# Performance work log

Hardware: AMD Instinct MI355X
Metric: run time of the kernel (lower is better)

Reference implementation:

```python
import jax, jax.numpy as jnp
from jax import lax
import numpy as np

B, H, W, C = 64, 224, 224, 3
OH, OW = 224, 224
EPS = 1e-3  # keras BatchNormalization default epsilon
FLAT = 52 * 52 * 10  # after conv7(valid)->pool2->conv5(valid)->pool2 on 224x224


def setup_inputs() -> dict:
    key = jax.random.key(0)
    ks = jax.random.split(key, 6)
    return {
        "x": jax.random.normal(ks[0], (B, H, W, C), jnp.float32),
        "c1_w": jax.random.normal(ks[1], (7, 7, C, 8), jnp.float32) * 0.05,
        "c1_b": jnp.zeros((8,), jnp.float32),
        "g1": jnp.ones((8,), jnp.float32),
        "b1": jnp.zeros((8,), jnp.float32),
        "m1": jnp.zeros((8,), jnp.float32),
        "v1": jnp.ones((8,), jnp.float32),
        "c2_w": jax.random.normal(ks[2], (5, 5, 8, 10), jnp.float32) * 0.05,
        "c2_b": jnp.zeros((10,), jnp.float32),
        "g2": jnp.ones((10,), jnp.float32),
        "b2": jnp.zeros((10,), jnp.float32),
        "m2": jnp.zeros((10,), jnp.float32),
        "v2": jnp.ones((10,), jnp.float32),
        "d1_w": jax.random.normal(ks[3], (FLAT, 32), jnp.float32) * 0.01,
        "d1_b": jnp.zeros((32,), jnp.float32),
        "d2_w": jax.random.normal(ks[4], (32, 6), jnp.float32) * 0.01,
        "d2_b": jnp.array([1.0, 0.0, 0.0, 0.0, 1.0, 0.0], jnp.float32),  # identity affine
    }


def _conv(x, w, b):
    return lax.conv_general_dilated(x, w, (1, 1), 'VALID',
                                    dimension_numbers=('NHWC', 'HWIO', 'NHWC')) + b


def _maxpool(x):
    return lax.reduce_window(x, -jnp.inf, lax.max, (1, 2, 2, 1), (1, 2, 2, 1), 'VALID')


def _bn(x, g, b, m, v):
    # inference-mode batchnorm: gamma*(x-mean)/sqrt(var+eps)+beta
    return (x - m) * lax.rsqrt(v + EPS) * g + b


def _bilinear(img, px, py):
    # img: [H,W,C]; px,py: [OH,OW] pixel-space sample coords; zero fill outside
    x0 = jnp.floor(px).astype(jnp.int32)
    y0 = jnp.floor(py).astype(jnp.int32)

    def gather(yi, xi):
        valid = (yi >= 0) & (yi < H) & (xi >= 0) & (xi < W)
        v = img[jnp.clip(yi, 0, H - 1), jnp.clip(xi, 0, W - 1)]  # [OH,OW,C]
        return v * valid[..., None]

    wx = (px - x0)[..., None]
    wy = (py - y0)[..., None]
    return (gather(y0, x0) * (1 - wx) * (1 - wy)
            + gather(y0, x0 + 1) * wx * (1 - wy)
            + gather(y0 + 1, x0) * (1 - wx) * wy
            + gather(y0 + 1, x0 + 1) * wx * wy)


def reference(x, c1_w, c1_b, g1, b1, m1, v1, c2_w, c2_b, g2, b2, m2, v2,
              d1_w, d1_b, d2_w, d2_b):
    # localization network
    h = _maxpool(_bn(jax.nn.relu(_conv(x, c1_w, c1_b)), g1, b1, m1, v1))
    h = _maxpool(_bn(jax.nn.relu(_conv(h, c2_w, c2_b)), g2, b2, m2, v2))
    h = h.reshape(h.shape[0], -1)                      # [B, FLAT]
    h = jax.nn.relu(h @ d1_w + d1_b)                   # [B, 32]
    theta = (h @ d2_w + d2_b).reshape(-1, 2, 3)        # [B, 2, 3]

    # normalized homogeneous grid [N,3] with N = OH*OW
    xs = jnp.linspace(-1.0, 1.0, OW)
    ys = jnp.linspace(-1.0, 1.0, OH)
    xg, yg = jnp.meshgrid(xs, ys)
    grid = jnp.stack([xg.ravel(), yg.ravel(), jnp.ones(OH * OW, jnp.float32)], axis=-1)

    coords = jnp.einsum('bij,nj->bni', theta, grid)    # [B, N, 2]
    px = ((coords[..., 0] + 1.0) * 0.5 * (W - 1)).reshape(-1, OH, OW)
    py = ((coords[..., 1] + 1.0) * 0.5 * (H - 1)).reshape(-1, OH, OW)
    return jax.vmap(_bilinear)(x, px, py)              # [B, OH, OW, C]
```

## Files before the change

### kernel.cpp

```cpp
#include <hip/hip_runtime.h>
#include <hip/hip_bf16.h>


#define NCHUNK 212
#define KC 128

__global__ __launch_bounds__(256) void k_conv1(
    const float* __restrict__ x, const float* __restrict__ w,
    const float* __restrict__ bias, const float* __restrict__ g,
    const float* __restrict__ bt, const float* __restrict__ m,
    const float* __restrict__ v, float* __restrict__ out) {
  __shared__ float s_in[3][38][42];
  __shared__ float s_bn[3][8];
  const int tid = threadIdx.x;
  const int bx = blockIdx.x, by = blockIdx.y, b = blockIdx.z;

  if (tid < 8) {
    float sc = g[tid] * rsqrtf(v[tid] + 1e-3f);
    s_bn[0][tid] = sc;
    s_bn[1][tid] = bt[tid] - m[tid] * sc;
    s_bn[2][tid] = bias[tid];
  }
  const int iy0 = by * 32, ix0 = bx * 32;
  const float* xb = x + (size_t)b * 224 * 224 * 3;
  for (int f = tid; f < 38 * 114; f += 256) {
    int r = f / 114, rem = f - r * 114;
    int q = rem / 3, c = rem - q * 3;
    int gy = iy0 + r; if (gy > 223) gy = 223;
    int gc = ix0 + q; if (gc > 223) gc = 223;
    s_in[c][r][q] = xb[(gy * 224 + gc) * 3 + c];
  }
  __syncthreads();

  const int pxl = tid & 15, pyl = tid >> 4;
  const int lx = 2 * pxl, ly = 2 * pyl;
  float acc[2][2][8];
#pragma unroll
  for (int pr = 0; pr < 2; ++pr)
#pragma unroll
    for (int pc = 0; pc < 2; ++pc)
#pragma unroll
      for (int co = 0; co < 8; ++co) acc[pr][pc][co] = 0.f;

#pragma unroll 1
  for (int ci = 0; ci < 3; ++ci) {
    float rw[8][8];
#pragma unroll
    for (int r = 0; r < 8; ++r)
#pragma unroll
      for (int j = 0; j < 4; ++j) {
        float2 t = *(const float2*)&s_in[ci][ly + r][lx + 2 * j];
        rw[r][2 * j] = t.x; rw[r][2 * j + 1] = t.y;
      }
#pragma unroll
    for (int ky = 0; ky < 7; ++ky) {
      float wv[7][8];
#pragma unroll
      for (int kx = 0; kx < 7; ++kx) {
        const float* wp = w + ((ky * 7 + kx) * 3 + ci) * 8;
        float4 a = *(const float4*)wp;
        float4 c4 = *(const float4*)(wp + 4);
        wv[kx][0] = a.x;  wv[kx][1] = a.y;  wv[kx][2] = a.z;  wv[kx][3] = a.w;
        wv[kx][4] = c4.x; wv[kx][5] = c4.y; wv[kx][6] = c4.z; wv[kx][7] = c4.w;
      }
#pragma unroll
      for (int kx = 0; kx < 7; ++kx)
#pragma unroll
        for (int pr = 0; pr < 2; ++pr)
#pragma unroll
          for (int pc = 0; pc < 2; ++pc) {
            float iv = rw[ky + pr][kx + pc];
#pragma unroll
            for (int co = 0; co < 8; ++co)
              acc[pr][pc][co] = fmaf(iv, wv[kx][co], acc[pr][pc][co]);
          }
    }
  }

  const int py = by * 16 + pyl, px = bx * 16 + pxl;
  if (py < 109 && px < 109) {
#pragma unroll
    for (int co = 0; co < 8; ++co) {
      float sc = s_bn[0][co], sh = s_bn[1][co], bs = s_bn[2][co];
      float a0 = fmaxf(acc[0][0][co] + bs, 0.f) * sc + sh;
      float a1 = fmaxf(acc[0][1][co] + bs, 0.f) * sc + sh;
      float a2 = fmaxf(acc[1][0][co] + bs, 0.f) * sc + sh;
      float a3 = fmaxf(acc[1][1][co] + bs, 0.f) * sc + sh;
      out[((size_t)co * 64 + b) * 109 * 110 + py * 110 + px] =
          fmaxf(fmaxf(a0, a1), fmaxf(a2, a3));
    }
  }
}

__global__ __launch_bounds__(256) void k_conv2(
    const float* __restrict__ in, const float* __restrict__ w,
    const float* __restrict__ bias, const float* __restrict__ g,
    const float* __restrict__ bt, const float* __restrict__ m,
    const float* __restrict__ v, float* __restrict__ out) {
  __shared__ float s_in[8][36][38];
  __shared__ float s_bn[3][10];
  const int tid = threadIdx.x;
  const int bx = blockIdx.x, by = blockIdx.y, b = blockIdx.z;

  if (tid < 10) {
    float sc = g[tid] * rsqrtf(v[tid] + 1e-3f);
    s_bn[0][tid] = sc;
    s_bn[1][tid] = bt[tid] - m[tid] * sc;
    s_bn[2][tid] = bias[tid];
  }
  const int iy0 = by * 32, ix0 = bx * 32;
  for (int f = tid; f < 8 * 36 * 36; f += 256) {
    int ci = f / 1296, rem = f - ci * 1296;
    int r = rem / 36, q = rem - r * 36;
    int gy = iy0 + r; if (gy > 108) gy = 108;
    int gc = ix0 + q; if (gc > 108) gc = 108;
    s_in[ci][r][q] = in[(((size_t)ci * 64 + b) * 109 + gy) * 110 + gc];
  }
  __syncthreads();

  const int pxl = tid & 15, pyl = tid >> 4;
  const int lx = 2 * pxl, ly = 2 * pyl;
  float acc[2][2][10];
#pragma unroll
  for (int pr = 0; pr < 2; ++pr)
#pragma unroll
    for (int pc = 0; pc < 2; ++pc)
#pragma unroll
      for (int co = 0; co < 10; ++co) acc[pr][pc][co] = 0.f;

#pragma unroll 1
  for (int ci = 0; ci < 8; ++ci) {
    float rw[6][8];
#pragma unroll
    for (int r = 0; r < 6; ++r)
#pragma unroll
      for (int j = 0; j < 4; ++j) {
        float2 t = *(const float2*)&s_in[ci][ly + r][lx + 2 * j];
        rw[r][2 * j] = t.x; rw[r][2 * j + 1] = t.y;
      }
#pragma unroll
    for (int ky = 0; ky < 5; ++ky) {
      float wv[5][10];
#pragma unroll
      for (int kx = 0; kx < 5; ++kx) {
        const float* wp = w + ((ky * 5 + kx) * 8 + ci) * 10;
#pragma unroll
        for (int u = 0; u < 5; ++u) {
          float2 t = *(const float2*)(wp + 2 * u);
          wv[kx][2 * u] = t.x; wv[kx][2 * u + 1] = t.y;
        }
      }
#pragma unroll
      for (int kx = 0; kx < 5; ++kx)
#pragma unroll
        for (int pr = 0; pr < 2; ++pr)
#pragma unroll
          for (int pc = 0; pc < 2; ++pc) {
            float iv = rw[ky + pr][kx + pc];
#pragma unroll
            for (int co = 0; co < 10; ++co)
              acc[pr][pc][co] = fmaf(iv, wv[kx][co], acc[pr][pc][co]);
          }
    }
  }

  const int py = by * 16 + pyl, px = bx * 16 + pxl;
  if (py < 52 && px < 52) {
    float res[10];
#pragma unroll
    for (int co = 0; co < 10; ++co) {
      float sc = s_bn[0][co], sh = s_bn[1][co], bs = s_bn[2][co];
      float a0 = fmaxf(acc[0][0][co] + bs, 0.f) * sc + sh;
      float a1 = fmaxf(acc[0][1][co] + bs, 0.f) * sc + sh;
      float a2 = fmaxf(acc[1][0][co] + bs, 0.f) * sc + sh;
      float a3 = fmaxf(acc[1][1][co] + bs, 0.f) * sc + sh;
      res[co] = fmaxf(fmaxf(a0, a1), fmaxf(a2, a3));
    }
    float2* op2 = (float2*)&out[(((size_t)b * 52 + py) * 52 + px) * 10];
#pragma unroll
    for (int i = 0; i < 5; i++)
      op2[i] = make_float2(res[2 * i], res[2 * i + 1]);
  }
}

__global__ __launch_bounds__(256) void k_fc1(
    const float* __restrict__ act, const float* __restrict__ w,
    float* __restrict__ partial) {
  __shared__ float s_w[KC * 32];
  __shared__ float s_a[64 * KC];
  const int tid = threadIdx.x;
  const int chunk = blockIdx.x;
  const int k0 = chunk * KC;
  for (int f = tid; f < KC * 32; f += 256) {
    int k = k0 + (f >> 5);
    s_w[f] = (k < 27040) ? w[(size_t)k0 * 32 + f] : 0.f;
  }
  for (int f = tid; f < 64 * KC; f += 256) {
    int bb = f >> 7, j = f & (KC - 1);
    int k = k0 + j;
    s_a[f] = (k < 27040) ? act[(size_t)bb * 27040 + k] : 0.f;
  }
  __syncthreads();
  const int o = tid & 31, bh = tid >> 5;
  float sums[8];
#pragma unroll
  for (int i = 0; i < 8; i++) sums[i] = 0.f;
#pragma unroll 1
  for (int j = 0; j < KC; j++) {
    float wv = s_w[j * 32 + o];
#pragma unroll
    for (int i = 0; i < 8; i++)
      sums[i] = fmaf(s_a[(i * 8 + bh) * KC + j], wv, sums[i]);
  }
#pragma unroll
  for (int i = 0; i < 8; i++)
    partial[(size_t)chunk * 2048 + i * 256 + tid] = sums[i];
}

__global__ __launch_bounds__(64) void k_fc2(
    const float* __restrict__ partial, const float* __restrict__ d1b,
    const float* __restrict__ d2w, const float* __restrict__ d2b,
    float* __restrict__ theta) {
  const int b = blockIdx.x;
  const int t = threadIdx.x;
  const int o = t & 31, half = t >> 5;
  float s = 0.f;
  const int c0 = half * (NCHUNK / 2), c1 = c0 + (NCHUNK / 2);
#pragma unroll 4
  for (int c = c0; c < c1; c++)
    s += partial[(size_t)c * 2048 + b * 32 + o];
  s += __shfl_down(s, 32);
  __shared__ float s_h[32];
  if (t < 32) s_h[o] = fmaxf(s + d1b[o], 0.f);
  __syncthreads();
  if (t < 6) {
    float th = d2b[t];
#pragma unroll
    for (int o2 = 0; o2 < 32; o2++) th = fmaf(s_h[o2], d2w[o2 * 6 + t], th);
    theta[b * 6 + t] = th;
  }
}

__global__ __launch_bounds__(256) void k_sample(
    const float* __restrict__ x, const float* __restrict__ theta,
    float* __restrict__ out) {
  const int b = blockIdx.y;
  __shared__ float th[6];
  if (threadIdx.x < 6) th[threadIdx.x] = theta[b * 6 + threadIdx.x];
  __syncthreads();
  const int t = blockIdx.x * 256 + threadIdx.x;
  const int oy = t / 224, ox = t - oy * 224;
  const float xn = -1.f + (2.f / 223.f) * (float)ox;
  const float yn = -1.f + (2.f / 223.f) * (float)oy;
  const float cx = th[0] * xn + th[1] * yn + th[2];
  const float cy = th[3] * xn + th[4] * yn + th[5];
  const float px = (cx + 1.f) * 0.5f * 223.f;
  const float py = (cy + 1.f) * 0.5f * 223.f;
  const float x0f = floorf(px), y0f = floorf(py);
  const int x0 = (int)x0f, y0 = (int)y0f;
  const float wx = px - x0f, wy = py - y0f;
  const float* xb = x + (size_t)b * 224 * 224 * 3;
  float a0 = 0.f, a1 = 0.f, a2 = 0.f;
#pragma unroll
  for (int dy = 0; dy < 2; dy++) {
    const int yi = y0 + dy;
    const bool vy = (yi >= 0) && (yi < 224);
    const int yc = yi < 0 ? 0 : (yi > 223 ? 223 : yi);
    const float wyv = dy ? wy : 1.f - wy;
#pragma unroll
    for (int dx = 0; dx < 2; dx++) {
      const int xi = x0 + dx;
      const bool vx = (xi >= 0) && (xi < 224);
      const int xc = xi < 0 ? 0 : (xi > 223 ? 223 : xi);
      const float wv = wyv * (dx ? wx : 1.f - wx) * ((vx && vy) ? 1.f : 0.f);
      const float* p = &xb[(yc * 224 + xc) * 3];
      a0 = fmaf(p[0], wv, a0);
      a1 = fmaf(p[1], wv, a1);
      a2 = fmaf(p[2], wv, a2);
    }
  }
  float* op = &out[((size_t)b * 50176 + t) * 3];
  op[0] = a0; op[1] = a1; op[2] = a2;
}

extern "C" void kernel_launch(void* const* d_in, const int* in_sizes, int n_in,
                              void* d_out, int out_size, void* d_ws, size_t ws_size,
                              hipStream_t stream) {
  const float* x    = (const float*)d_in[0];
  const float* c1w  = (const float*)d_in[1];
  const float* c1b  = (const float*)d_in[2];
  const float* g1   = (const float*)d_in[3];
  const float* b1   = (const float*)d_in[4];
  const float* m1   = (const float*)d_in[5];
  const float* v1   = (const float*)d_in[6];
  const float* c2w  = (const float*)d_in[7];
  const float* c2b  = (const float*)d_in[8];
  const float* g2   = (const float*)d_in[9];
  const float* b2   = (const float*)d_in[10];
  const float* m2   = (const float*)d_in[11];
  const float* v2   = (const float*)d_in[12];
  const float* d1w  = (const float*)d_in[13];
  const float* d1b  = (const float*)d_in[14];
  const float* d2w  = (const float*)d_in[15];
  const float* d2b  = (const float*)d_in[16];
  float* out = (float*)d_out;

  float* ws = (float*)d_ws;
  float* p1    = ws;
  float* p2    = p1 + 6138880;
  float* theta = p2 + 1730560;
  float* part  = ws;

  k_conv1<<<dim3(7, 7, 64), 256, 0, stream>>>(x, c1w, c1b, g1, b1, m1, v1, p1);
  k_conv2<<<dim3(4, 4, 64), 256, 0, stream>>>(p1, c2w, c2b, g2, b2, m2, v2, p2);
  k_fc1<<<NCHUNK, 256, 0, stream>>>(p2, d1w, part);
  k_fc2<<<64, 64, 0, stream>>>(part, d1b, d2w, d2b, theta);
  k_sample<<<dim3(196, 64), 256, 0, stream>>>(x, theta, out);
}
```

Baseline: 295.4 us.

## Process two images per conv1 block and retile FC1 reduction with vectorized loads

conv1 now handles two batch images per block, so each weight register load is reused across both images. Input rows are now loaded per ky rather than all at once, which cuts register pressure; launch bounds request 4 waves per SIMD. fc1 uses half-size K chunks (twice as many blocks) with float4 shared-memory reads and a new partial-sum layout, and fc2 reduces across 8 warp segments through shared memory. The risk is higher accumulator register use in conv1 and fewer conv1 blocks.

```diff
diff --git a/kernel.cpp b/kernel.cpp
--- a/kernel.cpp
+++ b/kernel.cpp
@@ -2,18 +2,19 @@
 #include <hip/hip_bf16.h>
 
 
-#define NCHUNK 212
-#define KC 128
-
-__global__ __launch_bounds__(256) void k_conv1(
+#define NCHUNK 423
+#define KC 64
+
+__global__ __launch_bounds__(256, 4) void k_conv1(
     const float* __restrict__ x, const float* __restrict__ w,
     const float* __restrict__ bias, const float* __restrict__ g,
     const float* __restrict__ bt, const float* __restrict__ m,
     const float* __restrict__ v, float* __restrict__ out) {
-  __shared__ float s_in[3][38][42];
+  __shared__ float s_in[2][3][38][42];
   __shared__ float s_bn[3][8];
   const int tid = threadIdx.x;
-  const int bx = blockIdx.x, by = blockIdx.y, b = blockIdx.z;
+  const int bx = blockIdx.x, by = blockIdx.y, z = blockIdx.z;
+  const int b0 = 2 * z;
 
   if (tid < 8) {
     float sc = g[tid] * rsqrtf(v[tid] + 1e-3f);
@@ -22,38 +23,40 @@
     s_bn[2][tid] = bias[tid];
   }
   const int iy0 = by * 32, ix0 = bx * 32;
-  const float* xb = x + (size_t)b * 224 * 224 * 3;
-  for (int f = tid; f < 38 * 114; f += 256) {
-    int r = f / 114, rem = f - r * 114;
-    int q = rem / 3, c = rem - q * 3;
+  for (int f = tid; f < 2 * 38 * 114; f += 256) {
+    int img = f / 4332, rem = f - img * 4332;
+    int r = rem / 114, rem2 = rem - r * 114;
+    int q = rem2 / 3, c = rem2 - q * 3;
     int gy = iy0 + r; if (gy > 223) gy = 223;
     int gc = ix0 + q; if (gc > 223) gc = 223;
-    s_in[c][r][q] = xb[(gy * 224 + gc) * 3 + c];
+    s_in[img][c][r][q] = x[((size_t)(b0 + img) * 224 + gy) * 224 * 3 + gc * 3 + c];
   }
   __syncthreads();
 
   const int pxl = tid & 15, pyl = tid >> 4;
   const int lx = 2 * pxl, ly = 2 * pyl;
-  float acc[2][2][8];
+  float accA[2][2][8], accB[2][2][8];
 #pragma unroll
   for (int pr = 0; pr < 2; ++pr)
 #pragma unroll
     for (int pc = 0; pc < 2; ++pc)
 #pragma unroll
-      for (int co = 0; co < 8; ++co) acc[pr][pc][co] = 0.f;
+      for (int co = 0; co < 8; ++co) { accA[pr][pc][co] = 0.f; accB[pr][pc][co] = 0.f; }
 
 #pragma unroll 1
   for (int ci = 0; ci < 3; ++ci) {
-    float rw[8][8];
-#pragma unroll
-    for (int r = 0; r < 8; ++r)
-#pragma unroll
-      for (int j = 0; j < 4; ++j) {
-        float2 t = *(const float2*)&s_in[ci][ly + r][lx + 2 * j];
-        rw[r][2 * j] = t.x; rw[r][2 * j + 1] = t.y;
-      }
-#pragma unroll
+#pragma unroll 1
     for (int ky = 0; ky < 7; ++ky) {
+      float rA[2][8], rB[2][8];
+#pragma unroll
+      for (int rr = 0; rr < 2; ++rr)
+#pragma unroll
+        for (int j = 0; j < 4; ++j) {
+          float2 ta = *(const float2*)&s_in[0][ci][ly + ky + rr][lx + 2 * j];
+          rA[rr][2 * j] = ta.x; rA[rr][2 * j + 1] = ta.y;
+          float2 tb = *(const float2*)&s_in[1][ci][ly + ky + rr][lx + 2 * j];
+          rB[rr][2 * j] = tb.x; rB[rr][2 * j + 1] = tb.y;
+        }
       float wv[7][8];
 #pragma unroll
       for (int kx = 0; kx < 7; ++kx) {
@@ -69,10 +72,13 @@
         for (int pr = 0; pr < 2; ++pr)
 #pragma unroll
           for (int pc = 0; pc < 2; ++pc) {
-            float iv = rw[ky + pr][kx + pc];
-#pragma unroll
-            for (int co = 0; co < 8; ++co)
-              acc[pr][pc][co] = fmaf(iv, wv[kx][co], acc[pr][pc][co]);
+            float ia = rA[pr][kx + pc];
+            float ib = rB[pr][kx + pc];
+#pragma unroll
+            for (int co = 0; co < 8; ++co) {
+              accA[pr][pc][co] = fmaf(ia, wv[kx][co], accA[pr][pc][co]);
+              accB[pr][pc][co] = fmaf(ib, wv[kx][co], accB[pr][pc][co]);
+            }
           }
     }
   }
@@ -82,12 +88,18 @@
 #pragma unroll
     for (int co = 0; co < 8; ++co) {
       float sc = s_bn[0][co], sh = s_bn[1][co], bs = s_bn[2][co];
-      float a0 = fmaxf(acc[0][0][co] + bs, 0.f) * sc + sh;
-      float a1 = fmaxf(acc[0][1][co] + bs, 0.f) * sc + sh;
-      float a2 = fmaxf(acc[1][0][co] + bs, 0.f) * sc + sh;
-      float a3 = fmaxf(acc[1][1][co] + bs, 0.f) * sc + sh;
-      out[((size_t)co * 64 + b) * 109 * 110 + py * 110 + px] =
+      float a0 = fmaxf(accA[0][0][co] + bs, 0.f) * sc + sh;
+      float a1 = fmaxf(accA[0][1][co] + bs, 0.f) * sc + sh;
+      float a2 = fmaxf(accA[1][0][co] + bs, 0.f) * sc + sh;
+      float a3 = fmaxf(accA[1][1][co] + bs, 0.f) * sc + sh;
+      out[((size_t)co * 64 + b0) * 109 * 110 + py * 110 + px] =
           fmaxf(fmaxf(a0, a1), fmaxf(a2, a3));
+      float c0 = fmaxf(accB[0][0][co] + bs, 0.f) * sc + sh;
+      float c1 = fmaxf(accB[0][1][co] + bs, 0.f) * sc + sh;
+      float c2 = fmaxf(accB[1][0][co] + bs, 0.f) * sc + sh;
+      float c3 = fmaxf(accB[1][1][co] + bs, 0.f) * sc + sh;
+      out[((size_t)co * 64 + b0 + 1) * 109 * 110 + py * 110 + px] =
+          fmaxf(fmaxf(c0, c1), fmaxf(c2, c3));
     }
   }
 }
@@ -186,52 +198,67 @@
 __global__ __launch_bounds__(256) void k_fc1(
     const float* __restrict__ act, const float* __restrict__ w,
     float* __restrict__ partial) {
+  __shared__ float s_a[64][KC];
   __shared__ float s_w[KC * 32];
-  __shared__ float s_a[64 * KC];
   const int tid = threadIdx.x;
   const int chunk = blockIdx.x;
   const int k0 = chunk * KC;
+  for (int f = tid; f < 64 * KC; f += 256) {
+    int row = f >> 6, j = f & (KC - 1);
+    int k = k0 + j;
+    s_a[row][j] = (k < 27040) ? act[(size_t)row * 27040 + k] : 0.f;
+  }
   for (int f = tid; f < KC * 32; f += 256) {
     int k = k0 + (f >> 5);
     s_w[f] = (k < 27040) ? w[(size_t)k0 * 32 + f] : 0.f;
   }
-  for (int f = tid; f < 64 * KC; f += 256) {
-    int bb = f >> 7, j = f & (KC - 1);
-    int k = k0 + j;
-    s_a[f] = (k < 27040) ? act[(size_t)bb * 27040 + k] : 0.f;
-  }
-  __syncthreads();
-  const int o = tid & 31, bh = tid >> 5;
+  __syncthreads();
+  const int o = tid & 31, gg = tid >> 5;
   float sums[8];
 #pragma unroll
   for (int i = 0; i < 8; i++) sums[i] = 0.f;
-#pragma unroll 1
-  for (int j = 0; j < KC; j++) {
-    float wv = s_w[j * 32 + o];
-#pragma unroll
-    for (int i = 0; i < 8; i++)
-      sums[i] = fmaf(s_a[(i * 8 + bh) * KC + j], wv, sums[i]);
+#pragma unroll 2
+  for (int j = 0; j < KC; j += 4) {
+    float w0 = s_w[j * 32 + o];
+    float w1 = s_w[(j + 1) * 32 + o];
+    float w2 = s_w[(j + 2) * 32 + o];
+    float w3 = s_w[(j + 3) * 32 + o];
+#pragma unroll
+    for (int i = 0; i < 8; i++) {
+      float4 av = *(const float4*)&s_a[gg * 8 + i][j];
+      sums[i] = fmaf(av.x, w0, sums[i]);
+      sums[i] = fmaf(av.y, w1, sums[i]);
+      sums[i] = fmaf(av.z, w2, sums[i]);
+      sums[i] = fmaf(av.w, w3, sums[i]);
+    }
   }
 #pragma unroll
   for (int i = 0; i < 8; i++)
-    partial[(size_t)chunk * 2048 + i * 256 + tid] = sums[i];
-}
-
-__global__ __launch_bounds__(64) void k_fc2(
+    partial[((size_t)chunk * 64 + gg * 8 + i) * 32 + o] = sums[i];
+}
+
+__global__ __launch_bounds__(256) void k_fc2(
     const float* __restrict__ partial, const float* __restrict__ d1b,
     const float* __restrict__ d2w, const float* __restrict__ d2b,
     float* __restrict__ theta) {
   const int b = blockIdx.x;
   const int t = threadIdx.x;
-  const int o = t & 31, half = t >> 5;
+  const int o = t & 31, seg = t >> 5;
+  const int c0 = (seg < 7) ? seg * 53 : 371;
+  const int cnt = (seg < 7) ? 53 : 52;
   float s = 0.f;
-  const int c0 = half * (NCHUNK / 2), c1 = c0 + (NCHUNK / 2);
-#pragma unroll 4
-  for (int c = c0; c < c1; c++)
-    s += partial[(size_t)c * 2048 + b * 32 + o];
-  s += __shfl_down(s, 32);
+  for (int c = c0; c < c0 + cnt; ++c)
+    s += partial[((size_t)c * 64 + b) * 32 + o];
+  __shared__ float s_red[8][33];
+  s_red[seg][o] = s;
+  __syncthreads();
   __shared__ float s_h[32];
-  if (t < 32) s_h[o] = fmaxf(s + d1b[o], 0.f);
+  if (t < 32) {
+    float tot = 0.f;
+#pragma unroll
+    for (int sg = 0; sg < 8; ++sg) tot += s_red[sg][t];
+    s_h[t] = fmaxf(tot + d1b[t], 0.f);
+  }
   __syncthreads();
   if (t < 6) {
     float th = d2b[t];
@@ -311,9 +338,9 @@
   float* theta = p2 + 1730560;
   float* part  = ws;
 
-  k_conv1<<<dim3(7, 7, 64), 256, 0, stream>>>(x, c1w, c1b, g1, b1, m1, v1, p1);
+  k_conv1<<<dim3(7, 7, 32), 256, 0, stream>>>(x, c1w, c1b, g1, b1, m1, v1, p1);
   k_conv2<<<dim3(4, 4, 64), 256, 0, stream>>>(p1, c2w, c2b, g2, b2, m2, v2, p2);
   k_fc1<<<NCHUNK, 256, 0, stream>>>(p2, d1w, part);
-  k_fc2<<<64, 64, 0, stream>>>(part, d1b, d2w, d2b, theta);
+  k_fc2<<<64, 256, 0, stream>>>(part, d1b, d2w, d2b, theta);
   k_sample<<<dim3(196, 64), 256, 0, stream>>>(x, theta, out);
 }
```

Result: no change. 299.3 us (+1.3%).
